# Kernel optimization log

Hardware: AMD Instinct MI355X
Metric: run time of the kernel (lower is better)

## Reference

```python
import jax, jax.numpy as jnp
import numpy as np

NEG_SLOPE = 0.2  # leaky_relu slope used by standard GAT attention


def _gat_layer(h, src, dst, W, a_src, a_dst, gru, n_nodes):
    """One gated multi-head GAT layer.
    h: [N, Din]; W: [H, Din, D]; a_src/a_dst: [H, D]; gru: None or (Wih,Whh,bih,bhh).
    Heads are merged by mean so output is [N, D].
    """
    Wh = jnp.einsum('nd,hdo->nho', h, W)                      # [N, H, D]
    es = jnp.einsum('nho,ho->nh', Wh, a_src)                  # [N, H]
    ed = jnp.einsum('nho,ho->nh', Wh, a_dst)                  # [N, H]
    e = jax.nn.leaky_relu(es[src] + ed[dst], NEG_SLOPE)       # [E, H]
    # edge softmax over each destination's in-neighborhood (segment softmax)
    m = jax.ops.segment_max(e, dst, num_segments=n_nodes)     # [N, H]
    w = jnp.exp(e - m[dst])                                   # [E, H]
    denom = jax.ops.segment_sum(w, dst, num_segments=n_nodes) # [N, H]
    alpha = w / denom[dst]                                    # [E, H]
    # gather-source / scatter-add aggregation
    agg = jax.ops.segment_sum(alpha[:, :, None] * Wh[src], dst,
                              num_segments=n_nodes)           # [N, H, D]
    out = jax.nn.elu(agg.mean(axis=1))                        # [N, D] (head-mean merge)
    if gru is not None:
        Wih, Whh, bih, bhh = gru
        gi = out @ Wih.T + bih                                # [N, 3D]
        gh = h @ Whh.T + bhh                                  # [N, 3D]
        ir, iz, in_ = jnp.split(gi, 3, axis=-1)
        hr, hz, hn = jnp.split(gh, 3, axis=-1)
        r = jax.nn.sigmoid(ir + hr)
        z = jax.nn.sigmoid(iz + hz)
        n = jnp.tanh(in_ + r * hn)
        out = (1.0 - z) * n + z * h                           # GRU-gated residual update
    return out


def setup_inputs() -> dict:
    N, E, D, H, OUT = 20000, 320000, 128, 4, 1
    key = jax.random.key(0)
    ks = jax.random.split(key, 24)
    sd = 1.0 / np.sqrt(D)
    inp = {
        'h': jax.random.normal(ks[0], (N, D), jnp.float32),
        'edge_index': jax.random.randint(ks[1], (2, E), 0, N, jnp.int64),
    }
    # GAT layers: layer1-3 have H heads, layer4 has 1 head
    heads = [H, H, H, 1]
    for i, hh in enumerate(heads, start=1):
        inp[f'W{i}'] = jax.random.normal(ks[2 + 3 * i], (hh, D, D), jnp.float32) * sd
        inp[f'as{i}'] = jax.random.normal(ks[3 + 3 * i], (hh, D), jnp.float32) * 0.1
        inp[f'ad{i}'] = jax.random.normal(ks[4 + 3 * i], (hh, D), jnp.float32) * 0.1
    # shared GRUSubLayer(hidden_dim) parameters (torch GRUCell layout)
    inp['Wih'] = jax.random.normal(ks[18], (3 * D, D), jnp.float32) * sd
    inp['Whh'] = jax.random.normal(ks[19], (3 * D, D), jnp.float32) * sd
    inp['bih'] = jnp.zeros((3 * D,), jnp.float32)
    inp['bhh'] = jnp.zeros((3 * D,), jnp.float32)
    # output head
    inp['W5'] = jax.random.normal(ks[20], (D, OUT), jnp.float32) * sd
    inp['b5'] = jnp.zeros((OUT,), jnp.float32)
    return inp


def reference(h, edge_index, W1, as1, ad1, W2, as2, ad2, W3, as3, ad3,
              W4, as4, ad4, Wih, Whh, bih, bhh, W5, b5):
    N = h.shape[0]
    src, dst = edge_index[0], edge_index[1]
    gru = (Wih, Whh, bih, bhh)
    h = _gat_layer(h, src, dst, W1, as1, ad1, None, N)   # require_gru=False
    h = _gat_layer(h, src, dst, W2, as2, ad2, gru, N)
    h = _gat_layer(h, src, dst, W3, as3, ad3, gru, N)
    h = _gat_layer(h, src, dst, W4, as4, ad4, gru, N)    # single head
    return jax.nn.sigmoid(h @ W5 + b5)                   # [N, out_dim]
```

## Files before the change

### kernel.cpp

```cpp
#include <hip/hip_runtime.h>
#include <math.h>

#define D 128

typedef __attribute__((ext_vector_type(8))) short bf16x8;
typedef __attribute__((ext_vector_type(4))) float f32x4;
typedef __attribute__((ext_vector_type(2))) float f32x2;

__device__ __forceinline__ float sigmoidf_(float x) { return 1.f / (1.f + __expf(-x)); }
__device__ __forceinline__ float u2f_lo(unsigned u) { return __uint_as_float(u << 16); }
__device__ __forceinline__ float u2f_hi(unsigned u) { return __uint_as_float(u & 0xffff0000u); }
__device__ __forceinline__ unsigned short f2b(float f) {
  unsigned u = __float_as_uint(f);
  return (unsigned short)((u + 0x7fffu + ((u >> 16) & 1u)) >> 16);
}
__device__ __forceinline__ float leaky_(float v) { return v > 0.f ? v : 0.2f * v; }

__device__ __forceinline__ void pack_post_elem(const float* __restrict__ W,
                                               unsigned short* __restrict__ Bp, int i, float scale) {
  int j = i & 7;
  int lane = (i >> 3) & 63;
  int rest = i >> 9;
  int db = rest & 7;
  int kb = rest >> 3;
  int k = kb * 32 + ((lane >> 4) << 3) + j;
  int d = db * 16 + (lane & 15);
  int h = k >> 7, kk = k & 127;
  Bp[i] = f2b(W[((size_t)h * 128 + kk) * 128 + d] * scale);
}
__device__ __forceinline__ void pack_gru_elem(const float* __restrict__ S,
                                              unsigned short* __restrict__ Bp, int i) {
  int j = i & 7;
  int lane = (i >> 3) & 63;
  int rest = i >> 9;
  int db = rest % 24;
  int kb = rest / 24;
  int k = kb * 32 + ((lane >> 4) << 3) + j;
  int col = db * 16 + (lane & 15);
  Bp[i] = f2b(S[(size_t)col * 128 + k]);
}

__global__ void __launch_bounds__(256) k_prep(const float* __restrict__ h0, unsigned short* __restrict__ h0b,
                                              const float* __restrict__ W1, const float* __restrict__ W2,
                                              const float* __restrict__ W3, const float* __restrict__ W4,
                                              const float* __restrict__ Wih, const float* __restrict__ Whh,
                                              unsigned short* __restrict__ B1, unsigned short* __restrict__ B2,
                                              unsigned short* __restrict__ B3, unsigned short* __restrict__ B4,
                                              unsigned short* __restrict__ Bih, unsigned short* __restrict__ Bhh,
                                              const float* __restrict__ as1, const float* __restrict__ ad1,
                                              const float* __restrict__ as2, const float* __restrict__ ad2,
                                              const float* __restrict__ as3, const float* __restrict__ ad3,
                                              const float* __restrict__ as4, const float* __restrict__ ad4,
                                              unsigned short* __restrict__ Pp1, float* __restrict__ Pf2,
                                              float* __restrict__ Pf3, float* __restrict__ Pf4,
                                              const int* __restrict__ dst, int* __restrict__ deg,
                                              int N, int E) {
  int i = blockIdx.x * 256 + threadIdx.x;
  const int NH = N * 128;
  if (i < NH) {
    h0b[i] = f2b(h0[i]);
    return;
  }
  i -= NH;
  if (i < 311296) {
    if (i < 65536) pack_post_elem(W1, B1, i, 0.25f);
    else if (i < 131072) pack_post_elem(W2, B2, i - 65536, 0.25f);
    else if (i < 196608) pack_post_elem(W3, B3, i - 131072, 0.25f);
    else if (i < 212992) pack_post_elem(W4, B4, i - 196608, 1.0f);
    else if (i < 262144) pack_gru_elem(Wih, Bih, i - 212992);
    else pack_gru_elem(Whh, Bhh, i - 262144);
    return;
  }
  i -= 311296;
  if (i < 2048) {
    int j = i & 7;
    int lane = (i >> 3) & 63;
    int kb = i >> 9;
    int k = kb * 32 + ((lane >> 4) << 3) + j;
    int col = lane & 15;
    float val = 0.f;
    if (col < 8) {
      int c = col >= 4;
      int h = c ? (col - 4) : col;
      const float* wrow = W1 + ((size_t)h * 128 + k) * 128;
      const float* av = (c ? ad1 : as1) + (size_t)h * 128;
      for (int d2 = 0; d2 < 128; ++d2) val += wrow[d2] * av[d2];
    }
    Pp1[i] = f2b(val);
    return;
  }
  i -= 2048;
  if (i < 3072) {
    int layer = i >> 10;
    int qq = i & 1023;
    int k = qq >> 3;
    int slot = qq & 7;
    const float *W, *as_, *ad_;
    float* out;
    int H;
    if (layer == 0) { W = W2; as_ = as2; ad_ = ad2; out = Pf2; H = 4; }
    else if (layer == 1) { W = W3; as_ = as3; ad_ = ad3; out = Pf3; H = 4; }
    else { W = W4; as_ = as4; ad_ = ad4; out = Pf4; H = 1; }
    int h = slot & 3;
    bool isEd = slot >= 4;
    float val = 0.f;
    if (h < H) {
      const float* wrow = W + ((size_t)h * 128 + k) * 128;
      const float* av = (isEd ? ad_ : as_) + (size_t)h * 128;
      for (int d2 = 0; d2 < 128; ++d2) val += wrow[d2] * av[d2];
    }
    out[qq] = val;
    return;
  }
  i -= 3072;
  if (i < E) atomicAdd(&deg[dst[i]], 1);
}

__global__ void __launch_bounds__(1024) k_scan(const int* __restrict__ deg, int* __restrict__ rowptr,
                                               int* __restrict__ fill, int N) {
  __shared__ int part[1024];
  const int tid = threadIdx.x;
  const int chunk = (N + 1023) / 1024;
  const int b = tid * chunk;
  const int e = min(N, b + chunk);
  int s = 0;
  for (int i = b; i < e; ++i) s += deg[i];
  part[tid] = s;
  __syncthreads();
  for (int off = 1; off < 1024; off <<= 1) {
    int v = (tid >= off) ? part[tid - off] : 0;
    __syncthreads();
    part[tid] += v;
    __syncthreads();
  }
  int run = (tid == 0) ? 0 : part[tid - 1];
  for (int i = b; i < e; ++i) {
    rowptr[i] = run;
    fill[i] = run;
    run += deg[i];
  }
  if (b < N && e == N) rowptr[N] = run;
}

__global__ void __launch_bounds__(256) k_scatter_esed(const int* __restrict__ src, const int* __restrict__ dst,
                                                      int* __restrict__ fill, int* __restrict__ srcs, int E,
                                                      const unsigned short* __restrict__ hb,
                                                      const unsigned short* __restrict__ Pp,
                                                      float* __restrict__ es, float* __restrict__ ed,
                                                      int N, int nS) {
  if ((int)blockIdx.x < nS) {
    int e = blockIdx.x * 256 + threadIdx.x;
    if (e < E) {
      int pos = atomicAdd(&fill[dst[e]], 1);
      srcs[pos] = src[e];
    }
    return;
  }
  const int blk = blockIdx.x - nS;
  const int w = threadIdx.x >> 6;
  const int lane = threadIdx.x & 63;
  const int r = lane & 15, g = lane >> 4;
  const int n0 = blk * 64 + w * 16;
  f32x4 acc = (f32x4)0.f;
  const int koff = g << 3;
#pragma unroll
  for (int kb = 0; kb < 4; ++kb) {
    int row = min(n0 + r, N - 1);
    bf16x8 a = *(const bf16x8*)&hb[(size_t)row * 128 + kb * 32 + koff];
    bf16x8 b = *(const bf16x8*)&Pp[((size_t)(kb * 64) + lane) * 8];
    acc = __builtin_amdgcn_mfma_f32_16x16x32_bf16(a, b, acc, 0, 0, 0);
  }
  const int rbase = n0 + g * 4;
#pragma unroll
  for (int i = 0; i < 4; ++i) {
    int row = rbase + i;
    if (row < N) {
      if (r < 4) es[(size_t)row * 4 + r] = acc[i];
      else if (r < 8) ed[(size_t)row * 4 + (r - 4)] = acc[i];
    }
  }
}

template <int H, int MODE>
__global__ void __launch_bounds__(512) k_layer(const int* __restrict__ rowptr,
                                               const int* __restrict__ srcs,
                                               const float* __restrict__ es,
                                               const float* __restrict__ ed,
                                               const unsigned short* __restrict__ hbG,
                                               const unsigned short* __restrict__ Bp,
                                               const float* __restrict__ hf,
                                               const unsigned short* __restrict__ Bih,
                                               const unsigned short* __restrict__ Bhh,
                                               const float* __restrict__ bih,
                                               const float* __restrict__ bhh,
                                               float* __restrict__ houtf,
                                               unsigned short* __restrict__ houtb,
                                               const float* __restrict__ Pf,
                                               float* __restrict__ eso, float* __restrict__ edo, int Hn,
                                               const float* __restrict__ W5,
                                               const float* __restrict__ b5,
                                               float* __restrict__ out) {
  constexpr int KD = H * 128;
  __shared__ unsigned short ts[16][KD + 8];
  __shared__ unsigned short xs[16][136];
  __shared__ float s_pr[16][8][8];
  __shared__ __align__(16) unsigned s_off[16][32];
  __shared__ __align__(16) float s_af[16][32][H == 1 ? 1 : 4];

  const int tid = threadIdx.x;
  const int n0 = blockIdx.x * 16;

  {
    const int slot = tid >> 5;
    const int t = n0 + slot;
    const int l = tid & 31;
    const int q = l & 15;
    const int eg = l >> 4;
    const int b0 = rowptr[t];
    const int deg = rowptr[t + 1] - b0;
    if (deg == 0) {
      if (l < 16) {
#pragma unroll
        for (int h = 0; h < H; ++h)
          *(uint4*)&ts[slot][h * 128 + q * 8] = make_uint4(0u, 0u, 0u, 0u);
      }
    } else {
      float edv[H];
#pragma unroll
      for (int h = 0; h < H; ++h) edv[h] = ed[(size_t)t * H + h];
      f32x2 acc[H][4];
#pragma unroll
      for (int h = 0; h < H; ++h)
#pragma unroll
        for (int j = 0; j < 4; ++j) acc[h][j] = (f32x2)0.f;
      const char* hbase = (const char*)hbG + q * 16;

      if (deg <= 32) {
        const bool act = l < deg;
        int s = 0;
        float vv[H];
        if (act) {
          s = srcs[b0 + l];
          if constexpr (H == 4) {
            float4 ev = *(const float4*)&es[(size_t)s * 4];
            vv[0] = leaky_(ev.x + edv[0]);
            vv[1] = leaky_(ev.y + edv[1]);
            vv[2] = leaky_(ev.z + edv[2]);
            vv[3] = leaky_(ev.w + edv[3]);
          } else {
            vv[0] = leaky_(es[s] + edv[0]);
          }
        } else {
#pragma unroll
          for (int h = 0; h < H; ++h) vv[h] = -1e30f;
        }
        float mv[H];
#pragma unroll
        for (int h = 0; h < H; ++h) mv[h] = vv[h];
#pragma unroll
        for (int off = 16; off; off >>= 1)
#pragma unroll
          for (int h = 0; h < H; ++h) mv[h] = fmaxf(mv[h], __shfl_xor(mv[h], off));
        float e[H], den[H];
#pragma unroll
        for (int h = 0; h < H; ++h) {
          e[h] = act ? __expf(vv[h] - mv[h]) : 0.f;
          den[h] = e[h];
        }
#pragma unroll
        for (int off = 16; off; off >>= 1)
#pragma unroll
          for (int h = 0; h < H; ++h) den[h] += __shfl_xor(den[h], off);
        s_off[slot][l] = act ? ((unsigned)s << 8) : 0u;
#pragma unroll
        for (int h = 0; h < H; ++h) s_af[slot][l][h] = e[h] * (1.f / den[h]);
        const int steps = (deg + 1) >> 1;
#pragma unroll 4
        for (int e2 = 0; e2 < steps; ++e2) {
          const int ei = e2 * 2 + eg;
          unsigned off = s_off[slot][ei];
          float af[H];
          if constexpr (H == 4) {
            float4 a4 = *(const float4*)&s_af[slot][ei][0];
            af[0] = a4.x; af[1] = a4.y; af[2] = a4.z; af[3] = a4.w;
          } else {
            af[0] = s_af[slot][ei][0];
          }
          uint4 v = *(const uint4*)(hbase + off);
          f32x2 vf0 = {u2f_lo(v.x), u2f_hi(v.x)};
          f32x2 vf1 = {u2f_lo(v.y), u2f_hi(v.y)};
          f32x2 vf2 = {u2f_lo(v.z), u2f_hi(v.z)};
          f32x2 vf3 = {u2f_lo(v.w), u2f_hi(v.w)};
#pragma unroll
          for (int h = 0; h < H; ++h) {
            f32x2 a2 = {af[h], af[h]};
            acc[h][0] += a2 * vf0;
            acc[h][1] += a2 * vf1;
            acc[h][2] += a2 * vf2;
            acc[h][3] += a2 * vf3;
          }
        }
      } else {
        float m[H], den[H], vreg[H];
        int sreg = 0;
#pragma unroll
        for (int h = 0; h < H; ++h) {
          m[h] = -1e30f;
          den[h] = 0.f;
          vreg[h] = -1e30f;
        }
        for (int i = l; i < deg; i += 32) {
          int s = srcs[b0 + i];
          float vv[H];
          if constexpr (H == 4) {
            float4 ev = *(const float4*)&es[(size_t)s * 4];
            vv[0] = ev.x + edv[0];
            vv[1] = ev.y + edv[1];
            vv[2] = ev.z + edv[2];
            vv[3] = ev.w + edv[3];
          } else {
            vv[0] = es[s] + edv[0];
          }
#pragma unroll
          for (int h = 0; h < H; ++h) {
            float v = leaky_(vv[h]);
            vv[h] = v;
            float nm = fmaxf(m[h], v);
            den[h] = den[h] * __expf(m[h] - nm) + __expf(v - nm);
            m[h] = nm;
          }
          if (i == l) {
            sreg = s;
#pragma unroll
            for (int h = 0; h < H; ++h) vreg[h] = vv[h];
          }
        }
#pragma unroll
        for (int off = 16; off; off >>= 1) {
#pragma unroll
          for (int h = 0; h < H; ++h) {
            float om = __shfl_xor(m[h], off);
            float od = __shfl_xor(den[h], off);
            float nm = fmaxf(m[h], om);
            den[h] = den[h] * __expf(m[h] - nm) + od * __expf(om - nm);
            m[h] = nm;
          }
        }
        float rden[H];
#pragma unroll
        for (int h = 0; h < H; ++h) rden[h] = 1.f / den[h];
        for (int c0 = 0; c0 < deg; c0 += 32) {
          const int ce = min(32, deg - c0);
          if (c0 == 0) {
            bool ok = l < deg;
            s_off[slot][l] = ok ? ((unsigned)sreg << 8) : 0u;
#pragma unroll
            for (int h = 0; h < H; ++h)
              s_af[slot][l][h] = ok ? (__expf(vreg[h] - m[h]) * rden[h]) : 0.f;
          } else {
            int i = c0 + l;
            bool ok = i < deg;
            int s = ok ? srcs[b0 + i] : 0;
            s_off[slot][l] = ok ? ((unsigned)s << 8) : 0u;
            float af[H];
#pragma unroll
            for (int h = 0; h < H; ++h) af[h] = 0.f;
            if (ok) {
              float vv[H];
              if constexpr (H == 4) {
                float4 ev = *(const float4*)&es[(size_t)s * 4];
                vv[0] = ev.x + edv[0];
                vv[1] = ev.y + edv[1];
                vv[2] = ev.z + edv[2];
                vv[3] = ev.w + edv[3];
              } else {
                vv[0] = es[s] + edv[0];
              }
#pragma unroll
              for (int h = 0; h < H; ++h)
                af[h] = __expf(leaky_(vv[h]) - m[h]) * rden[h];
            }
#pragma unroll
            for (int h = 0; h < H; ++h) s_af[slot][l][h] = af[h];
          }
          const int steps = (ce + 1) >> 1;
#pragma unroll 4
          for (int e2 = 0; e2 < steps; ++e2) {
            const int ei = e2 * 2 + eg;
            unsigned off = s_off[slot][ei];
            float af[H];
            if constexpr (H == 4) {
              float4 a4 = *(const float4*)&s_af[slot][ei][0];
              af[0] = a4.x; af[1] = a4.y; af[2] = a4.z; af[3] = a4.w;
            } else {
              af[0] = s_af[slot][ei][0];
            }
            uint4 v = *(const uint4*)(hbase + off);
            f32x2 vf0 = {u2f_lo(v.x), u2f_hi(v.x)};
            f32x2 vf1 = {u2f_lo(v.y), u2f_hi(v.y)};
            f32x2 vf2 = {u2f_lo(v.z), u2f_hi(v.z)};
            f32x2 vf3 = {u2f_lo(v.w), u2f_hi(v.w)};
#pragma unroll
            for (int h = 0; h < H; ++h) {
              f32x2 a2 = {af[h], af[h]};
              acc[h][0] += a2 * vf0;
              acc[h][1] += a2 * vf1;
              acc[h][2] += a2 * vf2;
              acc[h][3] += a2 * vf3;
            }
          }
        }
      }
#pragma unroll
      for (int h = 0; h < H; ++h)
#pragma unroll
        for (int j = 0; j < 4; ++j) {
          acc[h][j].x += __shfl_xor(acc[h][j].x, 16);
          acc[h][j].y += __shfl_xor(acc[h][j].y, 16);
        }
      if (l < 16) {
#pragma unroll
        for (int h = 0; h < H; ++h) {
          uint4 pk;
          pk.x = (unsigned)f2b(acc[h][0].x) | ((unsigned)f2b(acc[h][0].y) << 16);
          pk.y = (unsigned)f2b(acc[h][1].x) | ((unsigned)f2b(acc[h][1].y) << 16);
          pk.z = (unsigned)f2b(acc[h][2].x) | ((unsigned)f2b(acc[h][2].y) << 16);
          pk.w = (unsigned)f2b(acc[h][3].x) | ((unsigned)f2b(acc[h][3].y) << 16);
          *(uint4*)&ts[slot][h * 128 + q * 8] = pk;
        }
      }
    }
  }
  __syncthreads();

  const int w = tid >> 6;
  const int lane = tid & 63;
  const int r = lane & 15, g = lane >> 4;
  const int koff = g << 3;
  f32x4 pacc = (f32x4)0.f;
#pragma unroll
  for (int kb = 0; kb < KD / 32; ++kb) {
    bf16x8 a = *(const bf16x8*)&ts[r][kb * 32 + koff];
    bf16x8 b = *(const bf16x8*)&Bp[((size_t)(kb * 8 + w) * 64 + lane) * 8];
    pacc = __builtin_amdgcn_mfma_f32_16x16x32_bf16(a, b, pacc, 0, 0, 0);
  }
  const int col = w * 16 + r;

  if constexpr (MODE == 0) {
    float ps[4][8];
#pragma unroll
    for (int i = 0; i < 4; ++i)
#pragma unroll
      for (int c = 0; c < 8; ++c) ps[i][c] = 0.f;
    float4 pj0 = *(const float4*)&Pf[col * 8];
    float4 pj1 = *(const float4*)&Pf[col * 8 + 4];
#pragma unroll
    for (int i = 0; i < 4; ++i) {
      const int row = n0 + g * 4 + i;
      float o = pacc[i];
      o = o > 0.f ? o : expm1f(o);
      houtf[(size_t)row * 128 + col] = o;
      houtb[(size_t)row * 128 + col] = f2b(o);
      ps[i][0] += o * pj0.x; ps[i][1] += o * pj0.y;
      ps[i][2] += o * pj0.z; ps[i][3] += o * pj0.w;
      ps[i][4] += o * pj1.x; ps[i][5] += o * pj1.y;
      ps[i][6] += o * pj1.z; ps[i][7] += o * pj1.w;
    }
#pragma unroll
    for (int off = 1; off < 16; off <<= 1)
#pragma unroll
      for (int i = 0; i < 4; ++i)
#pragma unroll
        for (int c = 0; c < 8; ++c) ps[i][c] += __shfl_xor(ps[i][c], off);
    if (r == 0) {
#pragma unroll
      for (int i = 0; i < 4; ++i)
#pragma unroll
        for (int c = 0; c < 8; ++c) s_pr[g * 4 + i][c][w] = ps[i][c];
    }
    __syncthreads();
    if (tid < 128) {
      int row = tid >> 3;
      int c = tid & 7;
      float val = 0.f;
#pragma unroll
      for (int ww = 0; ww < 8; ++ww) val += s_pr[row][c][ww];
      int gr = n0 + row;
      if (c < 4) eso[(size_t)gr * 4 + c] = val;
      else edo[(size_t)gr * 4 + (c - 4)] = val;
    }
  } else {
#pragma unroll
    for (int i = 0; i < 4; ++i) {
      float o = pacc[i];
      o = o > 0.f ? o : expm1f(o);
      xs[g * 4 + i][col] = f2b(o);
    }
    __syncthreads();
    f32x4 ai[3], ah[3];
#pragma unroll
    for (int p = 0; p < 3; ++p) {
      ai[p] = (f32x4)0.f;
      ah[p] = (f32x4)0.f;
    }
#pragma unroll
    for (int kb = 0; kb < 4; ++kb) {
      bf16x8 ax = *(const bf16x8*)&xs[r][kb * 32 + koff];
      bf16x8 ahr = *(const bf16x8*)&hbG[(size_t)(n0 + r) * 128 + kb * 32 + koff];
#pragma unroll
      for (int p = 0; p < 3; ++p) {
        const int ct = p * 8 + w;
        bf16x8 bi = *(const bf16x8*)&Bih[((size_t)(kb * 24 + ct) * 64 + lane) * 8];
        bf16x8 bh = *(const bf16x8*)&Bhh[((size_t)(kb * 24 + ct) * 64 + lane) * 8];
        ai[p] = __builtin_amdgcn_mfma_f32_16x16x32_bf16(ax, bi, ai[p], 0, 0, 0);
        ah[p] = __builtin_amdgcn_mfma_f32_16x16x32_bf16(ahr, bh, ah[p], 0, 0, 0);
      }
    }
    const int j = col;
    const float bir = bih[j], biz = bih[128 + j], bin = bih[256 + j];
    const float bhr = bhh[j], bhz = bhh[128 + j], bhn = bhh[256 + j];
    if constexpr (MODE == 1) {
      float ps[4][8];
#pragma unroll
      for (int i = 0; i < 4; ++i)
#pragma unroll
        for (int c = 0; c < 8; ++c) ps[i][c] = 0.f;
      float4 pj0 = *(const float4*)&Pf[j * 8];
      float4 pj1 = *(const float4*)&Pf[j * 8 + 4];
#pragma unroll
      for (int i = 0; i < 4; ++i) {
        const int row = n0 + g * 4 + i;
        float rr = sigmoidf_(ai[0][i] + bir + ah[0][i] + bhr);
        float z = sigmoidf_(ai[1][i] + biz + ah[1][i] + bhz);
        float nn = tanhf(ai[2][i] + bin + rr * (ah[2][i] + bhn));
        float hp = hf[(size_t)row * 128 + j];
        float o = (1.f - z) * nn + z * hp;
        houtf[(size_t)row * 128 + j] = o;
        houtb[(size_t)row * 128 + j] = f2b(o);
        ps[i][0] += o * pj0.x; ps[i][1] += o * pj0.y;
        ps[i][2] += o * pj0.z; ps[i][3] += o * pj0.w;
        ps[i][4] += o * pj1.x; ps[i][5] += o * pj1.y;
        ps[i][6] += o * pj1.z; ps[i][7] += o * pj1.w;
      }
#pragma unroll
      for (int off = 1; off < 16; off <<= 1)
#pragma unroll
        for (int i = 0; i < 4; ++i)
#pragma unroll
          for (int c = 0; c < 8; ++c) ps[i][c] += __shfl_xor(ps[i][c], off);
      if (r == 0) {
#pragma unroll
        for (int i = 0; i < 4; ++i)
#pragma unroll
          for (int c = 0; c < 8; ++c) s_pr[g * 4 + i][c][w] = ps[i][c];
      }
      __syncthreads();
      if (tid < 128) {
        int row = tid >> 3;
        int c = tid & 7;
        float val = 0.f;
#pragma unroll
        for (int ww = 0; ww < 8; ++ww) val += s_pr[row][c][ww];
        int gr = n0 + row;
        if (c < Hn) eso[(size_t)gr * Hn + c] = val;
        else if (c >= 4 && c < 4 + Hn) edo[(size_t)gr * Hn + (c - 4)] = val;
      }
    } else {
      float pfin[4] = {0.f, 0.f, 0.f, 0.f};
      const float w5 = W5[j];
#pragma unroll
      for (int i = 0; i < 4; ++i) {
        const int row = n0 + g * 4 + i;
        float rr = sigmoidf_(ai[0][i] + bir + ah[0][i] + bhr);
        float z = sigmoidf_(ai[1][i] + biz + ah[1][i] + bhz);
        float nn = tanhf(ai[2][i] + bin + rr * (ah[2][i] + bhn));
        float hp = hf[(size_t)row * 128 + j];
        float o = (1.f - z) * nn + z * hp;
        pfin[i] += o * w5;
      }
#pragma unroll
      for (int off = 1; off < 16; off <<= 1)
#pragma unroll
        for (int i = 0; i < 4; ++i) pfin[i] += __shfl_xor(pfin[i], off);
      if (r == 0) {
#pragma unroll
        for (int i = 0; i < 4; ++i) s_pr[g * 4 + i][0][w] = pfin[i];
      }
      __syncthreads();
      if (tid < 16) {
        float s = b5[0];
#pragma unroll
        for (int ww = 0; ww < 8; ++ww) s += s_pr[tid][0][ww];
        out[n0 + tid] = sigmoidf_(s);
      }
    }
  }
}

extern "C" void kernel_launch(void* const* d_in, const int* in_sizes, int n_in,
                              void* d_out, int out_size, void* d_ws, size_t ws_size,
                              hipStream_t stream) {
  const float* h0 = (const float*)d_in[0];
  const int* ei = (const int*)d_in[1];
  const float* W1 = (const float*)d_in[2];
  const float* as1 = (const float*)d_in[3];
  const float* ad1 = (const float*)d_in[4];
  const float* W2 = (const float*)d_in[5];
  const float* as2 = (const float*)d_in[6];
  const float* ad2 = (const float*)d_in[7];
  const float* W3 = (const float*)d_in[8];
  const float* as3 = (const float*)d_in[9];
  const float* ad3 = (const float*)d_in[10];
  const float* W4 = (const float*)d_in[11];
  const float* as4 = (const float*)d_in[12];
  const float* ad4 = (const float*)d_in[13];
  const float* Wih = (const float*)d_in[14];
  const float* Whh = (const float*)d_in[15];
  const float* bih = (const float*)d_in[16];
  const float* bhh = (const float*)d_in[17];
  const float* W5 = (const float*)d_in[18];
  const float* b5 = (const float*)d_in[19];

  const int N = in_sizes[0] / D;
  const int E = in_sizes[1] / 2;
  const int* src = ei;
  const int* dst = ei + E;

  float* ws = (float*)d_ws;
  float* hA = ws;
  float* hB = hA + (size_t)N * 128;
  float* esA = hB + (size_t)N * 128;
  float* edA = esA + (size_t)N * 4;
  float* esB = edA + (size_t)N * 4;
  float* edB = esB + (size_t)N * 4;
  unsigned short* h0b = (unsigned short*)(edB + (size_t)N * 4);
  unsigned short* hAb = h0b + (size_t)N * 128;
  unsigned short* hBb = hAb + (size_t)N * 128;
  unsigned short* B1 = hBb + (size_t)N * 128;
  unsigned short* B2 = B1 + 65536;
  unsigned short* B3 = B2 + 65536;
  unsigned short* B4 = B3 + 65536;
  unsigned short* Bih = B4 + 16384;
  unsigned short* Bhh = Bih + 49152;
  unsigned short* Pp1 = Bhh + 49152;
  float* Pf2 = (float*)(Pp1 + 2048);
  float* Pf3 = Pf2 + 1024;
  float* Pf4 = Pf3 + 1024;
  int* deg = (int*)(Pf4 + 1024);
  int* rowptr = deg + N;
  int* fill = rowptr + N + 1;
  int* srcs = fill + N;

  hipMemsetAsync(deg, 0, (size_t)N * 4, stream);
  {
    const int total = N * 128 + 311296 + 2048 + 3072 + E;
    k_prep<<<(total + 255) / 256, 256, 0, stream>>>(
        h0, h0b, W1, W2, W3, W4, Wih, Whh, B1, B2, B3, B4, Bih, Bhh,
        as1, ad1, as2, ad2, as3, ad3, as4, ad4, Pp1, Pf2, Pf3, Pf4, dst, deg, N, E);
  }
  k_scan<<<1, 1024, 0, stream>>>(deg, rowptr, fill, N);
  {
    const int nS = (E + 255) / 256;
    const int nE = (N + 63) / 64;
    k_scatter_esed<<<nS + nE, 256, 0, stream>>>(src, dst, fill, srcs, E,
                                                h0b, Pp1, esA, edA, N, nS);
  }

  const int gL = N / 16;

  k_layer<4, 0><<<gL, 512, 0, stream>>>(rowptr, srcs, esA, edA, h0b, B1,
                                        nullptr, nullptr, nullptr, nullptr, nullptr,
                                        hA, hAb, Pf2, esB, edB, 4, nullptr, nullptr, nullptr);
  k_layer<4, 1><<<gL, 512, 0, stream>>>(rowptr, srcs, esB, edB, hAb, B2,
                                        hA, Bih, Bhh, bih, bhh,
                                        hB, hBb, Pf3, esA, edA, 4, nullptr, nullptr, nullptr);
  k_layer<4, 1><<<gL, 512, 0, stream>>>(rowptr, srcs, esA, edA, hBb, B3,
                                        hB, Bih, Bhh, bih, bhh,
                                        hA, hAb, Pf4, esB, edB, 1, nullptr, nullptr, nullptr);
  k_layer<1, 2><<<gL, 512, 0, stream>>>(rowptr, srcs, esB, edB, hAb, B4,
                                        hA, Bih, Bhh, bih, bhh,
                                        nullptr, nullptr, nullptr, nullptr, nullptr, 0,
                                        W5, b5, (float*)d_out);
}
```

Before: 262.6 us.

## Bucket nodes by in-degree so each layer block processes similar-degree nodes

The scan kernel now builds a degree histogram (capped at 63) and a counting-sort permutation of node ids by in-degree. Each layer kernel maps its 16 nodes per block through this order, so nodes with similar degree share a block. The goal is less load imbalance among the 32-lane slots within a block. In exchange, output rows are written to scattered locations and the extra loop inside the single-block scan adds serial work and shared-memory atomics.

```diff
diff --git a/kernel.cpp b/kernel.cpp
--- a/kernel.cpp
+++ b/kernel.cpp
@@ -117,8 +117,9 @@
 }
 
 __global__ void __launch_bounds__(1024) k_scan(const int* __restrict__ deg, int* __restrict__ rowptr,
-                                               int* __restrict__ fill, int N) {
+                                               int* __restrict__ fill, int* __restrict__ order, int N) {
   __shared__ int part[1024];
+  __shared__ int bh[64];
   const int tid = threadIdx.x;
   const int chunk = (N + 1023) / 1024;
   const int b = tid * chunk;
@@ -126,6 +127,7 @@
   int s = 0;
   for (int i = b; i < e; ++i) s += deg[i];
   part[tid] = s;
+  if (tid < 64) bh[tid] = 0;
   __syncthreads();
   for (int off = 1; off < 1024; off <<= 1) {
     int v = (tid >= off) ? part[tid - off] : 0;
@@ -138,8 +140,23 @@
     rowptr[i] = run;
     fill[i] = run;
     run += deg[i];
+    atomicAdd(&bh[min(deg[i], 63)], 1);
   }
   if (b < N && e == N) rowptr[N] = run;
+  __syncthreads();
+  if (tid == 0) {
+    int acc = 0;
+    for (int k = 0; k < 64; ++k) {
+      int c = bh[k];
+      bh[k] = acc;
+      acc += c;
+    }
+  }
+  __syncthreads();
+  for (int i = b; i < e; ++i) {
+    int pos = atomicAdd(&bh[min(deg[i], 63)], 1);
+    order[pos] = i;
+  }
 }
 
 __global__ void __launch_bounds__(256) k_scatter_esed(const int* __restrict__ src, const int* __restrict__ dst,
@@ -182,7 +199,8 @@
 }
 
 template <int H, int MODE>
-__global__ void __launch_bounds__(512) k_layer(const int* __restrict__ rowptr,
+__global__ void __launch_bounds__(512) k_layer(const int* __restrict__ order,
+                                               const int* __restrict__ rowptr,
                                                const int* __restrict__ srcs,
                                                const float* __restrict__ es,
                                                const float* __restrict__ ed,
@@ -206,13 +224,16 @@
   __shared__ float s_pr[16][8][8];
   __shared__ __align__(16) unsigned s_off[16][32];
   __shared__ __align__(16) float s_af[16][32][H == 1 ? 1 : 4];
+  __shared__ int s_ord[16];
 
   const int tid = threadIdx.x;
   const int n0 = blockIdx.x * 16;
+  if (tid < 16) s_ord[tid] = order[n0 + tid];
+  __syncthreads();
 
   {
     const int slot = tid >> 5;
-    const int t = n0 + slot;
+    const int t = s_ord[slot];
     const int l = tid & 31;
     const int q = l & 15;
     const int eg = l >> 4;
@@ -456,7 +477,7 @@
     float4 pj1 = *(const float4*)&Pf[col * 8 + 4];
 #pragma unroll
     for (int i = 0; i < 4; ++i) {
-      const int row = n0 + g * 4 + i;
+      const int row = s_ord[g * 4 + i];
       float o = pacc[i];
       o = o > 0.f ? o : expm1f(o);
       houtf[(size_t)row * 128 + col] = o;
@@ -485,7 +506,7 @@
       float val = 0.f;
 #pragma unroll
       for (int ww = 0; ww < 8; ++ww) val += s_pr[row][c][ww];
-      int gr = n0 + row;
+      int gr = s_ord[row];
       if (c < 4) eso[(size_t)gr * 4 + c] = val;
       else edo[(size_t)gr * 4 + (c - 4)] = val;
     }
@@ -503,10 +524,11 @@
       ai[p] = (f32x4)0.f;
       ah[p] = (f32x4)0.f;
     }
+    const int rowA = s_ord[r];
 #pragma unroll
     for (int kb = 0; kb < 4; ++kb) {
       bf16x8 ax = *(const bf16x8*)&xs[r][kb * 32 + koff];
-      bf16x8 ahr = *(const bf16x8*)&hbG[(size_t)(n0 + r) * 128 + kb * 32 + koff];
+      bf16x8 ahr = *(const bf16x8*)&hbG[(size_t)rowA * 128 + kb * 32 + koff];
 #pragma unroll
       for (int p = 0; p < 3; ++p) {
         const int ct = p * 8 + w;
@@ -529,7 +551,7 @@
       float4 pj1 = *(const float4*)&Pf[j * 8 + 4];
 #pragma unroll
       for (int i = 0; i < 4; ++i) {
-        const int row = n0 + g * 4 + i;
+        const int row = s_ord[g * 4 + i];
         float rr = sigmoidf_(ai[0][i] + bir + ah[0][i] + bhr);
         float z = sigmoidf_(ai[1][i] + biz + ah[1][i] + bhz);
         float nn = tanhf(ai[2][i] + bin + rr * (ah[2][i] + bhn));
@@ -561,7 +583,7 @@
         float val = 0.f;
 #pragma unroll
         for (int ww = 0; ww < 8; ++ww) val += s_pr[row][c][ww];
-        int gr = n0 + row;
+        int gr = s_ord[row];
         if (c < Hn) eso[(size_t)gr * Hn + c] = val;
         else if (c >= 4 && c < 4 + Hn) edo[(size_t)gr * Hn + (c - 4)] = val;
       }
@@ -570,7 +592,7 @@
       const float w5 = W5[j];
 #pragma unroll
       for (int i = 0; i < 4; ++i) {
-        const int row = n0 + g * 4 + i;
+        const int row = s_ord[g * 4 + i];
         float rr = sigmoidf_(ai[0][i] + bir + ah[0][i] + bhr);
         float z = sigmoidf_(ai[1][i] + biz + ah[1][i] + bhz);
         float nn = tanhf(ai[2][i] + bin + rr * (ah[2][i] + bhn));
@@ -591,7 +613,7 @@
         float s = b5[0];
 #pragma unroll
         for (int ww = 0; ww < 8; ++ww) s += s_pr[tid][0][ww];
-        out[n0 + tid] = sigmoidf_(s);
+        out[s_ord[tid]] = sigmoidf_(s);
       }
     }
   }
@@ -649,7 +671,8 @@
   int* deg = (int*)(Pf4 + 1024);
   int* rowptr = deg + N;
   int* fill = rowptr + N + 1;
-  int* srcs = fill + N;
+  int* order = fill + N;
+  int* srcs = order + N;
 
   hipMemsetAsync(deg, 0, (size_t)N * 4, stream);
   {
@@ -658,7 +681,7 @@
         h0, h0b, W1, W2, W3, W4, Wih, Whh, B1, B2, B3, B4, Bih, Bhh,
         as1, ad1, as2, ad2, as3, ad3, as4, ad4, Pp1, Pf2, Pf3, Pf4, dst, deg, N, E);
   }
-  k_scan<<<1, 1024, 0, stream>>>(deg, rowptr, fill, N);
+  k_scan<<<1, 1024, 0, stream>>>(deg, rowptr, fill, order, N);
   {
     const int nS = (E + 255) / 256;
     const int nE = (N + 63) / 64;
@@ -668,16 +691,16 @@
 
   const int gL = N / 16;
 
-  k_layer<4, 0><<<gL, 512, 0, stream>>>(rowptr, srcs, esA, edA, h0b, B1,
+  k_layer<4, 0><<<gL, 512, 0, stream>>>(order, rowptr, srcs, esA, edA, h0b, B1,
                                         nullptr, nullptr, nullptr, nullptr, nullptr,
                                         hA, hAb, Pf2, esB, edB, 4, nullptr, nullptr, nullptr);
-  k_layer<4, 1><<<gL, 512, 0, stream>>>(rowptr, srcs, esB, edB, hAb, B2,
+  k_layer<4, 1><<<gL, 512, 0, stream>>>(order, rowptr, srcs, esB, edB, hAb, B2,
                                         hA, Bih, Bhh, bih, bhh,
                                         hB, hBb, Pf3, esA, edA, 4, nullptr, nullptr, nullptr);
-  k_layer<4, 1><<<gL, 512, 0, stream>>>(rowptr, srcs, esA, edA, hBb, B3,
+  k_layer<4, 1><<<gL, 512, 0, stream>>>(order, rowptr, srcs, esA, edA, hBb, B3,
                                         hB, Bih, Bhh, bih, bhh,
                                         hA, hAb, Pf4, esB, edB, 1, nullptr, nullptr, nullptr);
-  k_layer<1, 2><<<gL, 512, 0, stream>>>(rowptr, srcs, esB, edB, hAb, B4,
+  k_layer<1, 2><<<gL, 512, 0, stream>>>(order, rowptr, srcs, esB, edB, hAb, B4,
                                         hA, Bih, Bhh, bih, bhh,
                                         nullptr, nullptr, nullptr, nullptr, nullptr, 0,
                                         W5, b5, (float*)d_out);
```

Result: slower. 282.0 us (+7.4%).

## Shrink layer blocks to 8 nodes and 256 threads, two column tiles per wave

Applied to the files above, without the earlier changes.

Each layer kernel now handles 8 destination nodes per block with 256 threads instead of 16 nodes with 512, which doubles the grid. Each of the 4 waves computes two 16-column MFMA tiles. The MFMA row dimension stays 16, so rows 8-15 duplicate rows 0-7 and are masked on store. The aim is smaller blocks, less LDS per block and more blocks to spread over CUs for the irregular gather phase, at the cost of half-wasted MFMA work and weight tiles reloaded across twice as many blocks.

```diff
diff --git a/kernel.cpp b/kernel.cpp
--- a/kernel.cpp
+++ b/kernel.cpp
@@ -182,7 +182,7 @@
 }
 
 template <int H, int MODE>
-__global__ void __launch_bounds__(512) k_layer(const int* __restrict__ rowptr,
+__global__ void __launch_bounds__(256) k_layer(const int* __restrict__ rowptr,
                                                const int* __restrict__ srcs,
                                                const float* __restrict__ es,
                                                const float* __restrict__ ed,
@@ -201,14 +201,14 @@
                                                const float* __restrict__ b5,
                                                float* __restrict__ out) {
   constexpr int KD = H * 128;
-  __shared__ unsigned short ts[16][KD + 8];
+  __shared__ unsigned short ts[8][KD + 8];
   __shared__ unsigned short xs[16][136];
-  __shared__ float s_pr[16][8][8];
-  __shared__ __align__(16) unsigned s_off[16][32];
-  __shared__ __align__(16) float s_af[16][32][H == 1 ? 1 : 4];
+  __shared__ float s_pr[8][8][4];
+  __shared__ __align__(16) unsigned s_off[8][32];
+  __shared__ __align__(16) float s_af[8][32][H == 1 ? 1 : 4];
 
   const int tid = threadIdx.x;
-  const int n0 = blockIdx.x * 16;
+  const int n0 = blockIdx.x * 8;
 
   {
     const int slot = tid >> 5;
@@ -437,14 +437,18 @@
   const int lane = tid & 63;
   const int r = lane & 15, g = lane >> 4;
   const int koff = g << 3;
-  f32x4 pacc = (f32x4)0.f;
+  f32x4 pacc[2];
+  pacc[0] = (f32x4)0.f;
+  pacc[1] = (f32x4)0.f;
 #pragma unroll
   for (int kb = 0; kb < KD / 32; ++kb) {
-    bf16x8 a = *(const bf16x8*)&ts[r][kb * 32 + koff];
-    bf16x8 b = *(const bf16x8*)&Bp[((size_t)(kb * 8 + w) * 64 + lane) * 8];
-    pacc = __builtin_amdgcn_mfma_f32_16x16x32_bf16(a, b, pacc, 0, 0, 0);
-  }
-  const int col = w * 16 + r;
+    bf16x8 a = *(const bf16x8*)&ts[r & 7][kb * 32 + koff];
+#pragma unroll
+    for (int t = 0; t < 2; ++t) {
+      bf16x8 b = *(const bf16x8*)&Bp[((size_t)(kb * 8 + w * 2 + t) * 64 + lane) * 8];
+      pacc[t] = __builtin_amdgcn_mfma_f32_16x16x32_bf16(a, b, pacc[t], 0, 0, 0);
+    }
+  }
 
   if constexpr (MODE == 0) {
     float ps[4][8];
@@ -452,96 +456,121 @@
     for (int i = 0; i < 4; ++i)
 #pragma unroll
       for (int c = 0; c < 8; ++c) ps[i][c] = 0.f;
-    float4 pj0 = *(const float4*)&Pf[col * 8];
-    float4 pj1 = *(const float4*)&Pf[col * 8 + 4];
-#pragma unroll
-    for (int i = 0; i < 4; ++i) {
-      const int row = n0 + g * 4 + i;
-      float o = pacc[i];
-      o = o > 0.f ? o : expm1f(o);
-      houtf[(size_t)row * 128 + col] = o;
-      houtb[(size_t)row * 128 + col] = f2b(o);
-      ps[i][0] += o * pj0.x; ps[i][1] += o * pj0.y;
-      ps[i][2] += o * pj0.z; ps[i][3] += o * pj0.w;
-      ps[i][4] += o * pj1.x; ps[i][5] += o * pj1.y;
-      ps[i][6] += o * pj1.z; ps[i][7] += o * pj1.w;
-    }
-#pragma unroll
-    for (int off = 1; off < 16; off <<= 1)
-#pragma unroll
-      for (int i = 0; i < 4; ++i)
-#pragma unroll
-        for (int c = 0; c < 8; ++c) ps[i][c] += __shfl_xor(ps[i][c], off);
-    if (r == 0) {
-#pragma unroll
-      for (int i = 0; i < 4; ++i)
-#pragma unroll
-        for (int c = 0; c < 8; ++c) s_pr[g * 4 + i][c][w] = ps[i][c];
-    }
-    __syncthreads();
-    if (tid < 128) {
-      int row = tid >> 3;
-      int c = tid & 7;
-      float val = 0.f;
-#pragma unroll
-      for (int ww = 0; ww < 8; ++ww) val += s_pr[row][c][ww];
-      int gr = n0 + row;
-      if (c < 4) eso[(size_t)gr * 4 + c] = val;
-      else edo[(size_t)gr * 4 + (c - 4)] = val;
-    }
-  } else {
-#pragma unroll
-    for (int i = 0; i < 4; ++i) {
-      float o = pacc[i];
-      o = o > 0.f ? o : expm1f(o);
-      xs[g * 4 + i][col] = f2b(o);
-    }
-    __syncthreads();
-    f32x4 ai[3], ah[3];
-#pragma unroll
-    for (int p = 0; p < 3; ++p) {
-      ai[p] = (f32x4)0.f;
-      ah[p] = (f32x4)0.f;
-    }
-#pragma unroll
-    for (int kb = 0; kb < 4; ++kb) {
-      bf16x8 ax = *(const bf16x8*)&xs[r][kb * 32 + koff];
-      bf16x8 ahr = *(const bf16x8*)&hbG[(size_t)(n0 + r) * 128 + kb * 32 + koff];
-#pragma unroll
-      for (int p = 0; p < 3; ++p) {
-        const int ct = p * 8 + w;
-        bf16x8 bi = *(const bf16x8*)&Bih[((size_t)(kb * 24 + ct) * 64 + lane) * 8];
-        bf16x8 bh = *(const bf16x8*)&Bhh[((size_t)(kb * 24 + ct) * 64 + lane) * 8];
-        ai[p] = __builtin_amdgcn_mfma_f32_16x16x32_bf16(ax, bi, ai[p], 0, 0, 0);
-        ah[p] = __builtin_amdgcn_mfma_f32_16x16x32_bf16(ahr, bh, ah[p], 0, 0, 0);
-      }
-    }
-    const int j = col;
-    const float bir = bih[j], biz = bih[128 + j], bin = bih[256 + j];
-    const float bhr = bhh[j], bhz = bhh[128 + j], bhn = bhh[256 + j];
-    if constexpr (MODE == 1) {
-      float ps[4][8];
-#pragma unroll
-      for (int i = 0; i < 4; ++i)
-#pragma unroll
-        for (int c = 0; c < 8; ++c) ps[i][c] = 0.f;
-      float4 pj0 = *(const float4*)&Pf[j * 8];
-      float4 pj1 = *(const float4*)&Pf[j * 8 + 4];
+#pragma unroll
+    for (int t = 0; t < 2; ++t) {
+      const int col = (w * 2 + t) * 16 + r;
+      float4 pj0 = *(const float4*)&Pf[col * 8];
+      float4 pj1 = *(const float4*)&Pf[col * 8 + 4];
 #pragma unroll
       for (int i = 0; i < 4; ++i) {
-        const int row = n0 + g * 4 + i;
-        float rr = sigmoidf_(ai[0][i] + bir + ah[0][i] + bhr);
-        float z = sigmoidf_(ai[1][i] + biz + ah[1][i] + bhz);
-        float nn = tanhf(ai[2][i] + bin + rr * (ah[2][i] + bhn));
-        float hp = hf[(size_t)row * 128 + j];
-        float o = (1.f - z) * nn + z * hp;
-        houtf[(size_t)row * 128 + j] = o;
-        houtb[(size_t)row * 128 + j] = f2b(o);
+        const int row8 = g * 4 + i;
+        float o = pacc[t][i];
+        o = o > 0.f ? o : expm1f(o);
+        if (row8 < 8) {
+          const int row = n0 + row8;
+          houtf[(size_t)row * 128 + col] = o;
+          houtb[(size_t)row * 128 + col] = f2b(o);
+        }
         ps[i][0] += o * pj0.x; ps[i][1] += o * pj0.y;
         ps[i][2] += o * pj0.z; ps[i][3] += o * pj0.w;
         ps[i][4] += o * pj1.x; ps[i][5] += o * pj1.y;
         ps[i][6] += o * pj1.z; ps[i][7] += o * pj1.w;
       }
+    }
+#pragma unroll
+    for (int off = 1; off < 16; off <<= 1)
+#pragma unroll
+      for (int i = 0; i < 4; ++i)
+#pragma unroll
+        for (int c = 0; c < 8; ++c) ps[i][c] += __shfl_xor(ps[i][c], off);
+    if (r == 0) {
+#pragma unroll
+      for (int i = 0; i < 4; ++i) {
+        const int row8 = g * 4 + i;
+        if (row8 < 8) {
+#pragma unroll
+          for (int c = 0; c < 8; ++c) s_pr[row8][c][w] = ps[i][c];
+        }
+      }
+    }
+    __syncthreads();
+    if (tid < 64) {
+      int row = tid >> 3;
+      int c = tid & 7;
+      float val = s_pr[row][c][0] + s_pr[row][c][1] + s_pr[row][c][2] + s_pr[row][c][3];
+      int gr = n0 + row;
+      if (c < 4) eso[(size_t)gr * 4 + c] = val;
+      else edo[(size_t)gr * 4 + (c - 4)] = val;
+    }
+  } else {
+#pragma unroll
+    for (int t = 0; t < 2; ++t) {
+      const int col = (w * 2 + t) * 16 + r;
+#pragma unroll
+      for (int i = 0; i < 4; ++i) {
+        float o = pacc[t][i];
+        o = o > 0.f ? o : expm1f(o);
+        xs[g * 4 + i][col] = f2b(o);
+      }
+    }
+    __syncthreads();
+    f32x4 ai[3][2], ah[3][2];
+#pragma unroll
+    for (int p = 0; p < 3; ++p)
+#pragma unroll
+      for (int t = 0; t < 2; ++t) {
+        ai[p][t] = (f32x4)0.f;
+        ah[p][t] = (f32x4)0.f;
+      }
+    const int rowA = n0 + (r & 7);
+#pragma unroll
+    for (int kb = 0; kb < 4; ++kb) {
+      bf16x8 ax = *(const bf16x8*)&xs[r][kb * 32 + koff];
+      bf16x8 ahr = *(const bf16x8*)&hbG[(size_t)rowA * 128 + kb * 32 + koff];
+#pragma unroll
+      for (int p = 0; p < 3; ++p) {
+#pragma unroll
+        for (int t = 0; t < 2; ++t) {
+          const int ct = p * 8 + w * 2 + t;
+          bf16x8 bi = *(const bf16x8*)&Bih[((size_t)(kb * 24 + ct) * 64 + lane) * 8];
+          bf16x8 bh = *(const bf16x8*)&Bhh[((size_t)(kb * 24 + ct) * 64 + lane) * 8];
+          ai[p][t] = __builtin_amdgcn_mfma_f32_16x16x32_bf16(ax, bi, ai[p][t], 0, 0, 0);
+          ah[p][t] = __builtin_amdgcn_mfma_f32_16x16x32_bf16(ahr, bh, ah[p][t], 0, 0, 0);
+        }
+      }
+    }
+    if constexpr (MODE == 1) {
+      float ps[4][8];
+#pragma unroll
+      for (int i = 0; i < 4; ++i)
+#pragma unroll
+        for (int c = 0; c < 8; ++c) ps[i][c] = 0.f;
+#pragma unroll
+      for (int t = 0; t < 2; ++t) {
+        const int j = (w * 2 + t) * 16 + r;
+        const float bir = bih[j], biz = bih[128 + j], bin = bih[256 + j];
+        const float bhr = bhh[j], bhz = bhh[128 + j], bhn = bhh[256 + j];
+        float4 pj0 = *(const float4*)&Pf[j * 8];
+        float4 pj1 = *(const float4*)&Pf[j * 8 + 4];
+#pragma unroll
+        for (int i = 0; i < 4; ++i) {
+          const int row8 = g * 4 + i;
+          const int row = n0 + (row8 & 7);
+          float rr = sigmoidf_(ai[0][t][i] + bir + ah[0][t][i] + bhr);
+          float z = sigmoidf_(ai[1][t][i] + biz + ah[1][t][i] + bhz);
+          float nn = tanhf(ai[2][t][i] + bin + rr * (ah[2][t][i] + bhn));
+          float hp = hf[(size_t)row * 128 + j];
+          float o = (1.f - z) * nn + z * hp;
+          if (row8 < 8) {
+            houtf[(size_t)row * 128 + j] = o;
+            houtb[(size_t)row * 128 + j] = f2b(o);
+          }
+          ps[i][0] += o * pj0.x; ps[i][1] += o * pj0.y;
+          ps[i][2] += o * pj0.z; ps[i][3] += o * pj0.w;
+          ps[i][4] += o * pj1.x; ps[i][5] += o * pj1.y;
+          ps[i][6] += o * pj1.z; ps[i][7] += o * pj1.w;
+        }
+      }
 #pragma unroll
       for (int off = 1; off < 16; off <<= 1)
 #pragma unroll
@@ -550,33 +579,42 @@
           for (int c = 0; c < 8; ++c) ps[i][c] += __shfl_xor(ps[i][c], off);
       if (r == 0) {
 #pragma unroll
-        for (int i = 0; i < 4; ++i)
-#pragma unroll
-          for (int c = 0; c < 8; ++c) s_pr[g * 4 + i][c][w] = ps[i][c];
+        for (int i = 0; i < 4; ++i) {
+          const int row8 = g * 4 + i;
+          if (row8 < 8) {
+#pragma unroll
+            for (int c = 0; c < 8; ++c) s_pr[row8][c][w] = ps[i][c];
+          }
+        }
       }
       __syncthreads();
-      if (tid < 128) {
+      if (tid < 64) {
         int row = tid >> 3;
         int c = tid & 7;
-        float val = 0.f;
-#pragma unroll
-        for (int ww = 0; ww < 8; ++ww) val += s_pr[row][c][ww];
+        float val = s_pr[row][c][0] + s_pr[row][c][1] + s_pr[row][c][2] + s_pr[row][c][3];
         int gr = n0 + row;
         if (c < Hn) eso[(size_t)gr * Hn + c] = val;
         else if (c >= 4 && c < 4 + Hn) edo[(size_t)gr * Hn + (c - 4)] = val;
       }
     } else {
       float pfin[4] = {0.f, 0.f, 0.f, 0.f};
-      const float w5 = W5[j];
-#pragma unroll
-      for (int i = 0; i < 4; ++i) {
-        const int row = n0 + g * 4 + i;
-        float rr = sigmoidf_(ai[0][i] + bir + ah[0][i] + bhr);
-        float z = sigmoidf_(ai[1][i] + biz + ah[1][i] + bhz);
-        float nn = tanhf(ai[2][i] + bin + rr * (ah[2][i] + bhn));
-        float hp = hf[(size_t)row * 128 + j];
-        float o = (1.f - z) * nn + z * hp;
-        pfin[i] += o * w5;
+#pragma unroll
+      for (int t = 0; t < 2; ++t) {
+        const int j = (w * 2 + t) * 16 + r;
+        const float bir = bih[j], biz = bih[128 + j], bin = bih[256 + j];
+        const float bhr = bhh[j], bhz = bhh[128 + j], bhn = bhh[256 + j];
+        const float w5 = W5[j];
+#pragma unroll
+        for (int i = 0; i < 4; ++i) {
+          const int row8 = g * 4 + i;
+          const int row = n0 + (row8 & 7);
+          float rr = sigmoidf_(ai[0][t][i] + bir + ah[0][t][i] + bhr);
+          float z = sigmoidf_(ai[1][t][i] + biz + ah[1][t][i] + bhz);
+          float nn = tanhf(ai[2][t][i] + bin + rr * (ah[2][t][i] + bhn));
+          float hp = hf[(size_t)row * 128 + j];
+          float o = (1.f - z) * nn + z * hp;
+          pfin[i] += o * w5;
+        }
       }
 #pragma unroll
       for (int off = 1; off < 16; off <<= 1)
@@ -584,13 +622,15 @@
         for (int i = 0; i < 4; ++i) pfin[i] += __shfl_xor(pfin[i], off);
       if (r == 0) {
 #pragma unroll
-        for (int i = 0; i < 4; ++i) s_pr[g * 4 + i][0][w] = pfin[i];
+        for (int i = 0; i < 4; ++i) {
+          const int row8 = g * 4 + i;
+          if (row8 < 8) s_pr[row8][0][w] = pfin[i];
+        }
       }
       __syncthreads();
-      if (tid < 16) {
-        float s = b5[0];
-#pragma unroll
-        for (int ww = 0; ww < 8; ++ww) s += s_pr[tid][0][ww];
+      if (tid < 8) {
+        float s = s_pr[tid][0][0] + s_pr[tid][0][1] +
+                  s_pr[tid][0][2] + s_pr[tid][0][3] + b5[0];
         out[n0 + tid] = sigmoidf_(s);
       }
     }
@@ -666,18 +706,18 @@
                                                 h0b, Pp1, esA, edA, N, nS);
   }
 
-  const int gL = N / 16;
-
-  k_layer<4, 0><<<gL, 512, 0, stream>>>(rowptr, srcs, esA, edA, h0b, B1,
+  const int gL = N / 8;
+
+  k_layer<4, 0><<<gL, 256, 0, stream>>>(rowptr, srcs, esA, edA, h0b, B1,
                                         nullptr, nullptr, nullptr, nullptr, nullptr,
                                         hA, hAb, Pf2, esB, edB, 4, nullptr, nullptr, nullptr);
-  k_layer<4, 1><<<gL, 512, 0, stream>>>(rowptr, srcs, esB, edB, hAb, B2,
+  k_layer<4, 1><<<gL, 256, 0, stream>>>(rowptr, srcs, esB, edB, hAb, B2,
                                         hA, Bih, Bhh, bih, bhh,
                                         hB, hBb, Pf3, esA, edA, 4, nullptr, nullptr, nullptr);
-  k_layer<4, 1><<<gL, 512, 0, stream>>>(rowptr, srcs, esA, edA, hBb, B3,
+  k_layer<4, 1><<<gL, 256, 0, stream>>>(rowptr, srcs, esA, edA, hBb, B3,
                                         hB, Bih, Bhh, bih, bhh,
                                         hA, hAb, Pf4, esB, edB, 1, nullptr, nullptr, nullptr);
-  k_layer<1, 2><<<gL, 512, 0, stream>>>(rowptr, srcs, esB, edB, hAb, B4,
+  k_layer<1, 2><<<gL, 256, 0, stream>>>(rowptr, srcs, esB, edB, hAb, B4,
                                         hA, Bih, Bhh, bih, bhh,
                                         nullptr, nullptr, nullptr, nullptr, nullptr, 0,
                                         W5, b5, (float*)d_out);
```

Result: slower. 348.2 us (+32.6%).
